# Optimization experiments

Measured on AMD Instinct MI355X. Metric: run time of the kernel, lower is better.

Reference implementation:

```python
import jax, jax.numpy as jnp
import numpy as np

N_NODES = 50000
N_EDGES = 800000
IN_F = 128
OUT_F = 64
ALPHA = 0.2  # LeakyReLU negative slope


def setup_inputs() -> dict:
    key = jax.random.key(0)
    k_h, k_e, k_w, k_b, k_a = jax.random.split(key, 5)
    h = jax.random.normal(k_h, (N_NODES, IN_F), dtype=jnp.float32)
    adj = jax.random.randint(k_e, (2, N_EDGES), 0, N_NODES, dtype=jnp.int64)
    # Linear(in_features, out_features): weight [out, in], bias [out]
    W_w = jax.random.normal(k_w, (OUT_F, IN_F), dtype=jnp.float32) * (1.0 / np.sqrt(IN_F))
    W_b = jax.random.normal(k_b, (OUT_F,), dtype=jnp.float32) * 0.01
    a = jax.random.normal(k_a, (1, 2 * OUT_F), dtype=jnp.float32) * (1.0 / np.sqrt(2 * OUT_F))
    return {"h": h, "adj": adj, "W_w": W_w, "W_b": W_b, "a": a}


def reference(h, adj, W_w, W_b, a):
    N = h.shape[0]
    F_out = W_w.shape[0]
    inv_sqrt_f = 1.0 / float(np.sqrt(F_out))

    data = h @ W_w.T + W_b                      # [N, F_out]
    src, dst = adj[0], adj[1]

    # a @ [data[src] || data[dst]]^T  == (data @ a_src)[src] + (data @ a_dst)[dst]
    a_src, a_dst = a[0, :F_out], a[0, F_out:]
    score = (data @ a_src)[src] + (data @ a_dst)[dst]       # [E]
    edge_e = jnp.exp(jax.nn.leaky_relu(score, ALPHA) * inv_sqrt_f)

    # sparse rowsum over source rows (duplicate edges sum, matching COO semantics)
    rowsum = jax.ops.segment_sum(edge_e, src, num_segments=N)  # [N]
    row_zero = rowsum == 0.0
    rowsum = jnp.where(row_zero, 1.0, rowsum)

    # sparse mm: sum_e edge_e * data[dst] into row src; zero rows get a unit self-loop
    h_prime = jax.ops.segment_sum(edge_e[:, None] * data[dst], src, num_segments=N)
    h_prime = h_prime + row_zero[:, None].astype(data.dtype) * data
    return h_prime / rowsum[:, None]
```

## Files before the change

kernel.cpp:

```cpp
#include <hip/hip_runtime.h>
#include <math.h>

#define IN_F 128
#define OUT_F 64
#define ALPHA 0.2f
#define INV_SQRT_F 0.125f
#define CAP 64
#define BINSH 7
#define BINSZ 128
#define CAPB 4096

typedef _Float16 h8  __attribute__((ext_vector_type(8)));
typedef float    f4  __attribute__((ext_vector_type(4)));

__device__ __forceinline__ float edge_w(float sc) {
    float lr = sc > 0.f ? sc : ALPHA * sc;
    return __expf(lr * INV_SQRT_F);
}

__device__ __forceinline__ h8 cvt8(float4 a, float4 b) {
    h8 r;
    r[0] = (_Float16)a.x; r[1] = (_Float16)a.y;
    r[2] = (_Float16)a.z; r[3] = (_Float16)a.w;
    r[4] = (_Float16)b.x; r[5] = (_Float16)b.y;
    r[6] = (_Float16)b.z; r[7] = (_Float16)b.w;
    return r;
}

__global__ __launch_bounds__(256) void k_p1(
    const float* __restrict__ h, const float* __restrict__ W,
    const float* __restrict__ b, const float* __restrict__ a,
    const int* __restrict__ src, const int* __restrict__ dst,
    int* __restrict__ gcur, unsigned* __restrict__ pk,
    _Float16* __restrict__ data_h,
    float* __restrict__ s_src, float* __restrict__ s_dst,
    int n_nodes, int n_edges, int g_lin)
{
    __shared__ int hist[512];
    __shared__ int off[512];
    const int tid = threadIdx.x;

    if ((int)blockIdx.x >= g_lin) {
        const int nbins = (n_nodes + BINSZ - 1) >> BINSH;
        const int e0 = ((int)blockIdx.x - g_lin) * 4096 + tid * 16;

        for (int i = tid; i < nbins; i += 256) hist[i] = 0;
        __syncthreads();

        int s[16], d[16];
        const bool full = (e0 + 16 <= n_edges);
        if (full) {
            #pragma unroll
            for (int c = 0; c < 4; ++c) {
                int4 s4 = *(const int4*)&src[e0 + c * 4];
                int4 d4 = *(const int4*)&dst[e0 + c * 4];
                s[c*4+0] = s4.x; s[c*4+1] = s4.y; s[c*4+2] = s4.z; s[c*4+3] = s4.w;
                d[c*4+0] = d4.x; d[c*4+1] = d4.y; d[c*4+2] = d4.z; d[c*4+3] = d4.w;
            }
            #pragma unroll
            for (int i = 0; i < 16; ++i)
                atomicAdd(&hist[s[i] >> BINSH], 1);
        } else {
            #pragma unroll
            for (int i = 0; i < 16; ++i) {
                int e = e0 + i;
                s[i] = (e < n_edges) ? src[e] : -1;
                d[i] = (e < n_edges) ? dst[e] : 0;
                if (s[i] >= 0) atomicAdd(&hist[s[i] >> BINSH], 1);
            }
        }
        __syncthreads();

        for (int i = tid; i < nbins; i += 256) {
            int c = hist[i];
            off[i] = (c > 0) ? atomicAdd(&gcur[i], c) : 0;
            hist[i] = 0;
        }
        __syncthreads();

        #pragma unroll
        for (int i = 0; i < 16; ++i) {
            if (s[i] < 0) continue;
            int bin = s[i] >> BINSH;
            int r = atomicAdd(&hist[bin], 1);
            int p = off[bin] + r;
            if (p < CAPB)
                pk[(size_t)bin * CAPB + p] =
                    ((unsigned)(s[i] & (BINSZ - 1)) << 16) | (unsigned)d[i];
        }
        return;
    }

    const int node0 = (int)blockIdx.x * 64;
    const int wv  = tid >> 6;
    const int lane = tid & 63;
    const int q   = lane >> 4;
    const int col = lane & 15;
    const int r0  = wv * 16;

    const int arow = min(node0 + r0 + col, n_nodes - 1);
    const float* __restrict__ hrow = h + (size_t)arow * IN_F;

    f4 acc[4] = {{0.f,0.f,0.f,0.f},{0.f,0.f,0.f,0.f},
                 {0.f,0.f,0.f,0.f},{0.f,0.f,0.f,0.f}};
    #pragma unroll
    for (int kk = 0; kk < 4; ++kk) {
        const int ko = kk * 32 + q * 8;
        float4 ha = *(const float4*)&hrow[ko];
        float4 hb = *(const float4*)&hrow[ko + 4];
        h8 av = cvt8(ha, hb);
        #pragma unroll
        for (int ct = 0; ct < 4; ++ct) {
            const float* wrow = W + (size_t)(ct * 16 + col) * IN_F + ko;
            float4 wa = *(const float4*)&wrow[0];
            float4 wb = *(const float4*)&wrow[4];
            h8 bv = cvt8(wa, wb);
            acc[ct] = __builtin_amdgcn_mfma_f32_16x16x32_f16(av, bv, acc[ct], 0, 0, 0);
        }
    }

    float bb[4], as_[4], ad_[4];
    #pragma unroll
    for (int ct = 0; ct < 4; ++ct) {
        bb[ct]  = b[ct * 16 + col];
        as_[ct] = a[ct * 16 + col];
        ad_[ct] = a[OUT_F + ct * 16 + col];
    }
    #pragma unroll
    for (int reg = 0; reg < 4; ++reg) {
        int n = node0 + r0 + q * 4 + reg;
        float vv[4], ps = 0.f, pd = 0.f;
        #pragma unroll
        for (int ct = 0; ct < 4; ++ct) {
            float v = acc[ct][reg] + bb[ct];
            vv[ct] = v;
            ps = fmaf(v, as_[ct], ps);
            pd = fmaf(v, ad_[ct], pd);
        }
        #pragma unroll
        for (int m = 1; m <= 8; m <<= 1) {
            ps += __shfl_xor(ps, m, 64);
            pd += __shfl_xor(pd, m, 64);
        }
        if (n < n_nodes) {
            size_t base = (size_t)n * OUT_F + col;
            #pragma unroll
            for (int ct = 0; ct < 4; ++ct)
                data_h[base + ct * 16] = (_Float16)vv[ct];
            if (col == 0) { s_src[n] = ps; s_dst[n] = pd; }
        }
    }
}

__global__ __launch_bounds__(256) void k_p2(
    const unsigned* __restrict__ pk, const int* __restrict__ gcur,
    unsigned short* __restrict__ db, int* __restrict__ cnt, int n_nodes)
{
    __shared__ unsigned short dbl[BINSZ * CAP];
    __shared__ int lcnt[BINSZ];
    const int b = blockIdx.x, tid = threadIdx.x;

    for (int i = tid; i < BINSZ; i += 256) lcnt[i] = 0;
    __syncthreads();

    const int ecnt = min(gcur[b], CAPB);
    for (int i = tid; i < ecnt; i += 256) {
        unsigned v = pk[(size_t)b * CAPB + i];
        int sl = (int)(v >> 16);
        int r = atomicAdd(&lcnt[sl], 1);
        if (r < CAP) dbl[sl * CAP + r] = (unsigned short)(v & 0xffffu);
    }
    __syncthreads();

    const int sbase = b * BINSZ;
    for (int i = tid; i < BINSZ; i += 256) {
        int s = sbase + i;
        if (s < n_nodes) cnt[s] = lcnt[i];
    }
    unsigned* dbu = (unsigned*)db;
    const unsigned* dbl32 = (const unsigned*)dbl;
    const size_t obase = (size_t)b * (BINSZ * CAP / 2);
    for (int i = tid; i < BINSZ * CAP / 2; i += 256)
        __builtin_nontemporal_store(dbl32[i], &dbu[obase + i]);
}

__global__ __launch_bounds__(256) void k_gather(
    const unsigned short* __restrict__ db, const int* __restrict__ cnt,
    const float* __restrict__ s_src, const float* __restrict__ s_dst,
    const _Float16* __restrict__ data_h, float* __restrict__ out, int n_nodes)
{
    const int wv = threadIdx.x >> 6, lane = threadIdx.x & 63;
    const int n = blockIdx.x * 4 + wv;
    if (n >= n_nodes) return;
    const int cn = min(cnt[n], CAP);
    const int g  = lane >> 3;
    const int fl = lane & 7;
    const float ssrc = s_src[n];
    const size_t bbase = (size_t)n * CAP;

    float ac[8] = {0.f,0.f,0.f,0.f,0.f,0.f,0.f,0.f};
    float rs = 0.f;
    int t = 0;
    for (; t + 16 <= cn; t += 16) {
        int d0 = (int)db[bbase + t + g];
        int d1 = (int)db[bbase + t + 8 + g];
        float w0 = edge_w(ssrc + s_dst[d0]);
        float w1 = edge_w(ssrc + s_dst[d1]);
        h8 x0 = *(const h8*)&data_h[(size_t)d0 * OUT_F + 8 * fl];
        h8 x1 = *(const h8*)&data_h[(size_t)d1 * OUT_F + 8 * fl];
        #pragma unroll
        for (int i = 0; i < 8; ++i) ac[i] = fmaf(w0, (float)x0[i], ac[i]);
        #pragma unroll
        for (int i = 0; i < 8; ++i) ac[i] = fmaf(w1, (float)x1[i], ac[i]);
        rs += w0 + w1;
    }
    for (; t + 8 <= cn; t += 8) {
        int d0 = (int)db[bbase + t + g];
        float w0 = edge_w(ssrc + s_dst[d0]);
        h8 x0 = *(const h8*)&data_h[(size_t)d0 * OUT_F + 8 * fl];
        #pragma unroll
        for (int i = 0; i < 8; ++i) ac[i] = fmaf(w0, (float)x0[i], ac[i]);
        rs += w0;
    }
    const int rem = cn - t;
    if (g < rem) {
        int d0 = (int)db[bbase + t + g];
        float w0 = edge_w(ssrc + s_dst[d0]);
        h8 x0 = *(const h8*)&data_h[(size_t)d0 * OUT_F + 8 * fl];
        #pragma unroll
        for (int i = 0; i < 8; ++i) ac[i] = fmaf(w0, (float)x0[i], ac[i]);
        rs += w0;
    }
    #pragma unroll
    for (int m = 8; m <= 32; m <<= 1) {
        #pragma unroll
        for (int i = 0; i < 8; ++i) ac[i] += __shfl_xor(ac[i], m, 64);
        rs += __shfl_xor(rs, m, 64);
    }

    if (g == 0) {
        size_t o = (size_t)n * OUT_F + 8 * fl;
        f4 r0, r1;
        if (rs == 0.f) {
            h8 xv = *(const h8*)&data_h[o];
            r0[0] = (float)xv[0]; r0[1] = (float)xv[1];
            r0[2] = (float)xv[2]; r0[3] = (float)xv[3];
            r1[0] = (float)xv[4]; r1[1] = (float)xv[5];
            r1[2] = (float)xv[6]; r1[3] = (float)xv[7];
        } else {
            float inv = 1.f / rs;
            r0[0] = ac[0] * inv; r0[1] = ac[1] * inv;
            r0[2] = ac[2] * inv; r0[3] = ac[3] * inv;
            r1[0] = ac[4] * inv; r1[1] = ac[5] * inv;
            r1[2] = ac[6] * inv; r1[3] = ac[7] * inv;
        }
        __builtin_nontemporal_store(r0, (f4*)&out[o]);
        __builtin_nontemporal_store(r1, (f4*)&out[o + 4]);
    }
}

extern "C" void kernel_launch(void* const* d_in, const int* in_sizes, int n_in,
                              void* d_out, int out_size, void* d_ws, size_t ws_size,
                              hipStream_t stream)
{
    const float* h   = (const float*)d_in[0];
    const int*   adj = (const int*)  d_in[1];
    const float* W   = (const float*)d_in[2];
    const float* b   = (const float*)d_in[3];
    const float* a   = (const float*)d_in[4];
    float* out = (float*)d_out;

    const int n_nodes = in_sizes[0] / IN_F;
    const int n_edges = in_sizes[1] / 2;
    const int* src = adj;
    const int* dst = adj + n_edges;
    const int nbins = (n_nodes + BINSZ - 1) >> BINSH;

    char* p = (char*)d_ws;
    _Float16*       data_h = (_Float16*)p;       p += (size_t)n_nodes * OUT_F * 2;
    unsigned short* db     = (unsigned short*)p; p += (size_t)nbins * BINSZ * CAP * 2;
    unsigned*       pk     = (unsigned*)p;       p += (size_t)nbins * CAPB * 4;
    float*          s_src  = (float*)p;          p += (size_t)n_nodes * 4;
    float*          s_dst  = (float*)p;          p += (size_t)n_nodes * 4;
    int*            cnt    = (int*)p;            p += (size_t)n_nodes * 4;
    int*            gcur   = (int*)p;            p += (size_t)nbins * 4;

    (void)hipMemsetAsync(gcur, 0, (size_t)nbins * sizeof(int), stream);

    const int g_lin = (n_nodes + 63) / 64;
    const int g_p1  = (n_edges + 4095) / 4096;
    k_p1<<<g_lin + g_p1, 256, 0, stream>>>(
        h, W, b, a, src, dst, gcur, pk, data_h, s_src, s_dst,
        n_nodes, n_edges, g_lin);

    k_p2<<<nbins, 256, 0, stream>>>(pk, gcur, db, cnt, n_nodes);

    k_gather<<<(n_nodes + 3) / 4, 256, 0, stream>>>(
        db, cnt, s_src, s_dst, data_h, out, n_nodes);
}
```

Measured before the change: 132.4 us.

## Fuse bin scatter and gather into one kernel with LDS-resident adjacency

Merges the per-bin bucketing kernel and the per-node gather kernel so each 1024-thread block builds its bin's adjacency lists in shared memory and immediately aggregates the 128 nodes from there. This removes the global write and reread of the padded neighbor list and count arrays and one kernel launch. The linear-projection blocks now stage W converted to fp16 in LDS, and edge-binning blocks are ordered first. The risk is reduced parallelism in the gather phase, since there are only a few hundred large blocks processing nodes serially per wave.

Measured after the change: 124.8 us. 5.7% less time.

```diff
diff --git a/kernel.cpp b/kernel.cpp
--- a/kernel.cpp
+++ b/kernel.cpp
@@ -9,6 +9,7 @@
 #define BINSH 7
 #define BINSZ 128
 #define CAPB 4096
+#define HS 136
 
 typedef _Float16 h8  __attribute__((ext_vector_type(8)));
 typedef float    f4  __attribute__((ext_vector_type(4)));
@@ -34,15 +35,16 @@
     int* __restrict__ gcur, unsigned* __restrict__ pk,
     _Float16* __restrict__ data_h,
     float* __restrict__ s_src, float* __restrict__ s_dst,
-    int n_nodes, int n_edges, int g_lin)
+    int n_nodes, int n_edges, int g_p1)
 {
+    __shared__ _Float16 wsh[OUT_F * HS];
     __shared__ int hist[512];
     __shared__ int off[512];
     const int tid = threadIdx.x;
 
-    if ((int)blockIdx.x >= g_lin) {
+    if ((int)blockIdx.x < g_p1) {
         const int nbins = (n_nodes + BINSZ - 1) >> BINSH;
-        const int e0 = ((int)blockIdx.x - g_lin) * 4096 + tid * 16;
+        const int e0 = (int)blockIdx.x * 4096 + tid * 16;
 
         for (int i = tid; i < nbins; i += 256) hist[i] = 0;
         __syncthreads();
@@ -91,7 +93,16 @@
         return;
     }
 
-    const int node0 = (int)blockIdx.x * 64;
+    const int node0 = ((int)blockIdx.x - g_p1) * 64;
+
+    for (int i = tid * 8; i < OUT_F * IN_F; i += 2048) {
+        int f = i >> 7, k = i & 127;
+        float4 va = *(const float4*)&W[i];
+        float4 vb = *(const float4*)&W[i + 4];
+        *(h8*)&wsh[f * HS + k] = cvt8(va, vb);
+    }
+    __syncthreads();
+
     const int wv  = tid >> 6;
     const int lane = tid & 63;
     const int q   = lane >> 4;
@@ -111,10 +122,7 @@
         h8 av = cvt8(ha, hb);
         #pragma unroll
         for (int ct = 0; ct < 4; ++ct) {
-            const float* wrow = W + (size_t)(ct * 16 + col) * IN_F + ko;
-            float4 wa = *(const float4*)&wrow[0];
-            float4 wb = *(const float4*)&wrow[4];
-            h8 bv = cvt8(wa, wb);
+            h8 bv = *(const h8*)&wsh[(ct * 16 + col) * HS + ko];
             acc[ct] = __builtin_amdgcn_mfma_f32_16x16x32_f16(av, bv, acc[ct], 0, 0, 0);
         }
     }
@@ -152,110 +160,99 @@
     }
 }
 
-__global__ __launch_bounds__(256) void k_p2(
+__global__ __launch_bounds__(1024) void k_bin(
     const unsigned* __restrict__ pk, const int* __restrict__ gcur,
-    unsigned short* __restrict__ db, int* __restrict__ cnt, int n_nodes)
+    const float* __restrict__ s_src, const float* __restrict__ s_dst,
+    const _Float16* __restrict__ data_h, float* __restrict__ out, int n_nodes)
 {
     __shared__ unsigned short dbl[BINSZ * CAP];
     __shared__ int lcnt[BINSZ];
-    const int b = blockIdx.x, tid = threadIdx.x;
-
-    for (int i = tid; i < BINSZ; i += 256) lcnt[i] = 0;
+    const int bin = blockIdx.x, tid = threadIdx.x;
+
+    for (int i = tid; i < BINSZ; i += 1024) lcnt[i] = 0;
     __syncthreads();
 
-    const int ecnt = min(gcur[b], CAPB);
-    for (int i = tid; i < ecnt; i += 256) {
-        unsigned v = pk[(size_t)b * CAPB + i];
+    const int ecnt = min(gcur[bin], CAPB);
+    for (int i = tid; i < ecnt; i += 1024) {
+        unsigned v = pk[(size_t)bin * CAPB + i];
         int sl = (int)(v >> 16);
         int r = atomicAdd(&lcnt[sl], 1);
         if (r < CAP) dbl[sl * CAP + r] = (unsigned short)(v & 0xffffu);
     }
     __syncthreads();
 
-    const int sbase = b * BINSZ;
-    for (int i = tid; i < BINSZ; i += 256) {
-        int s = sbase + i;
-        if (s < n_nodes) cnt[s] = lcnt[i];
-    }
-    unsigned* dbu = (unsigned*)db;
-    const unsigned* dbl32 = (const unsigned*)dbl;
-    const size_t obase = (size_t)b * (BINSZ * CAP / 2);
-    for (int i = tid; i < BINSZ * CAP / 2; i += 256)
-        __builtin_nontemporal_store(dbl32[i], &dbu[obase + i]);
-}
-
-__global__ __launch_bounds__(256) void k_gather(
-    const unsigned short* __restrict__ db, const int* __restrict__ cnt,
-    const float* __restrict__ s_src, const float* __restrict__ s_dst,
-    const _Float16* __restrict__ data_h, float* __restrict__ out, int n_nodes)
-{
-    const int wv = threadIdx.x >> 6, lane = threadIdx.x & 63;
-    const int n = blockIdx.x * 4 + wv;
-    if (n >= n_nodes) return;
-    const int cn = min(cnt[n], CAP);
+    const int wv = tid >> 6, lane = tid & 63;
     const int g  = lane >> 3;
     const int fl = lane & 7;
-    const float ssrc = s_src[n];
-    const size_t bbase = (size_t)n * CAP;
-
-    float ac[8] = {0.f,0.f,0.f,0.f,0.f,0.f,0.f,0.f};
-    float rs = 0.f;
-    int t = 0;
-    for (; t + 16 <= cn; t += 16) {
-        int d0 = (int)db[bbase + t + g];
-        int d1 = (int)db[bbase + t + 8 + g];
-        float w0 = edge_w(ssrc + s_dst[d0]);
-        float w1 = edge_w(ssrc + s_dst[d1]);
-        h8 x0 = *(const h8*)&data_h[(size_t)d0 * OUT_F + 8 * fl];
-        h8 x1 = *(const h8*)&data_h[(size_t)d1 * OUT_F + 8 * fl];
-        #pragma unroll
-        for (int i = 0; i < 8; ++i) ac[i] = fmaf(w0, (float)x0[i], ac[i]);
-        #pragma unroll
-        for (int i = 0; i < 8; ++i) ac[i] = fmaf(w1, (float)x1[i], ac[i]);
-        rs += w0 + w1;
-    }
-    for (; t + 8 <= cn; t += 8) {
-        int d0 = (int)db[bbase + t + g];
-        float w0 = edge_w(ssrc + s_dst[d0]);
-        h8 x0 = *(const h8*)&data_h[(size_t)d0 * OUT_F + 8 * fl];
-        #pragma unroll
-        for (int i = 0; i < 8; ++i) ac[i] = fmaf(w0, (float)x0[i], ac[i]);
-        rs += w0;
-    }
-    const int rem = cn - t;
-    if (g < rem) {
-        int d0 = (int)db[bbase + t + g];
-        float w0 = edge_w(ssrc + s_dst[d0]);
-        h8 x0 = *(const h8*)&data_h[(size_t)d0 * OUT_F + 8 * fl];
-        #pragma unroll
-        for (int i = 0; i < 8; ++i) ac[i] = fmaf(w0, (float)x0[i], ac[i]);
-        rs += w0;
-    }
-    #pragma unroll
-    for (int m = 8; m <= 32; m <<= 1) {
-        #pragma unroll
-        for (int i = 0; i < 8; ++i) ac[i] += __shfl_xor(ac[i], m, 64);
-        rs += __shfl_xor(rs, m, 64);
-    }
-
-    if (g == 0) {
-        size_t o = (size_t)n * OUT_F + 8 * fl;
-        f4 r0, r1;
-        if (rs == 0.f) {
-            h8 xv = *(const h8*)&data_h[o];
-            r0[0] = (float)xv[0]; r0[1] = (float)xv[1];
-            r0[2] = (float)xv[2]; r0[3] = (float)xv[3];
-            r1[0] = (float)xv[4]; r1[1] = (float)xv[5];
-            r1[2] = (float)xv[6]; r1[3] = (float)xv[7];
-        } else {
-            float inv = 1.f / rs;
-            r0[0] = ac[0] * inv; r0[1] = ac[1] * inv;
-            r0[2] = ac[2] * inv; r0[3] = ac[3] * inv;
-            r1[0] = ac[4] * inv; r1[1] = ac[5] * inv;
-            r1[2] = ac[6] * inv; r1[3] = ac[7] * inv;
-        }
-        __builtin_nontemporal_store(r0, (f4*)&out[o]);
-        __builtin_nontemporal_store(r1, (f4*)&out[o + 4]);
+
+    #pragma unroll 1
+    for (int ni = 0; ni < 8; ++ni) {
+        const int nl = wv * 8 + ni;
+        const int n = bin * BINSZ + nl;
+        if (n >= n_nodes) break;
+        const int cn = min(lcnt[nl], CAP);
+        const float ssrc = s_src[n];
+        const int bbase = nl * CAP;
+
+        float ac[8] = {0.f,0.f,0.f,0.f,0.f,0.f,0.f,0.f};
+        float rs = 0.f;
+        int t = 0;
+        for (; t + 16 <= cn; t += 16) {
+            int d0 = (int)dbl[bbase + t + g];
+            int d1 = (int)dbl[bbase + t + 8 + g];
+            float w0 = edge_w(ssrc + s_dst[d0]);
+            float w1 = edge_w(ssrc + s_dst[d1]);
+            h8 x0 = *(const h8*)&data_h[(size_t)d0 * OUT_F + 8 * fl];
+            h8 x1 = *(const h8*)&data_h[(size_t)d1 * OUT_F + 8 * fl];
+            #pragma unroll
+            for (int i = 0; i < 8; ++i) ac[i] = fmaf(w0, (float)x0[i], ac[i]);
+            #pragma unroll
+            for (int i = 0; i < 8; ++i) ac[i] = fmaf(w1, (float)x1[i], ac[i]);
+            rs += w0 + w1;
+        }
+        for (; t + 8 <= cn; t += 8) {
+            int d0 = (int)dbl[bbase + t + g];
+            float w0 = edge_w(ssrc + s_dst[d0]);
+            h8 x0 = *(const h8*)&data_h[(size_t)d0 * OUT_F + 8 * fl];
+            #pragma unroll
+            for (int i = 0; i < 8; ++i) ac[i] = fmaf(w0, (float)x0[i], ac[i]);
+            rs += w0;
+        }
+        const int rem = cn - t;
+        if (g < rem) {
+            int d0 = (int)dbl[bbase + t + g];
+            float w0 = edge_w(ssrc + s_dst[d0]);
+            h8 x0 = *(const h8*)&data_h[(size_t)d0 * OUT_F + 8 * fl];
+            #pragma unroll
+            for (int i = 0; i < 8; ++i) ac[i] = fmaf(w0, (float)x0[i], ac[i]);
+            rs += w0;
+        }
+        #pragma unroll
+        for (int m = 8; m <= 32; m <<= 1) {
+            #pragma unroll
+            for (int i = 0; i < 8; ++i) ac[i] += __shfl_xor(ac[i], m, 64);
+            rs += __shfl_xor(rs, m, 64);
+        }
+
+        if (g == 0) {
+            size_t o = (size_t)n * OUT_F + 8 * fl;
+            f4 r0, r1;
+            if (rs == 0.f) {
+                h8 xv = *(const h8*)&data_h[o];
+                r0[0] = (float)xv[0]; r0[1] = (float)xv[1];
+                r0[2] = (float)xv[2]; r0[3] = (float)xv[3];
+                r1[0] = (float)xv[4]; r1[1] = (float)xv[5];
+                r1[2] = (float)xv[6]; r1[3] = (float)xv[7];
+            } else {
+                float inv = 1.f / rs;
+                r0[0] = ac[0] * inv; r0[1] = ac[1] * inv;
+                r0[2] = ac[2] * inv; r0[3] = ac[3] * inv;
+                r1[0] = ac[4] * inv; r1[1] = ac[5] * inv;
+                r1[2] = ac[6] * inv; r1[3] = ac[7] * inv;
+            }
+            __builtin_nontemporal_store(r0, (f4*)&out[o]);
+            __builtin_nontemporal_store(r1, (f4*)&out[o + 4]);
+        }
     }
 }
 
@@ -278,23 +275,19 @@
 
     char* p = (char*)d_ws;
     _Float16*       data_h = (_Float16*)p;       p += (size_t)n_nodes * OUT_F * 2;
-    unsigned short* db     = (unsigned short*)p; p += (size_t)nbins * BINSZ * CAP * 2;
     unsigned*       pk     = (unsigned*)p;       p += (size_t)nbins * CAPB * 4;
     float*          s_src  = (float*)p;          p += (size_t)n_nodes * 4;
     float*          s_dst  = (float*)p;          p += (size_t)n_nodes * 4;
-    int*            cnt    = (int*)p;            p += (size_t)n_nodes * 4;
     int*            gcur   = (int*)p;            p += (size_t)nbins * 4;
 
     (void)hipMemsetAsync(gcur, 0, (size_t)nbins * sizeof(int), stream);
 
+    const int g_p1  = (n_edges + 4095) / 4096;
     const int g_lin = (n_nodes + 63) / 64;
-    const int g_p1  = (n_edges + 4095) / 4096;
-    k_p1<<<g_lin + g_p1, 256, 0, stream>>>(
+    k_p1<<<g_p1 + g_lin, 256, 0, stream>>>(
         h, W, b, a, src, dst, gcur, pk, data_h, s_src, s_dst,
-        n_nodes, n_edges, g_lin);
-
-    k_p2<<<nbins, 256, 0, stream>>>(pk, gcur, db, cnt, n_nodes);
-
-    k_gather<<<(n_nodes + 3) / 4, 256, 0, stream>>>(
-        db, cnt, s_src, s_dst, data_h, out, n_nodes);
-}
+        n_nodes, n_edges, g_p1);
+
+    k_bin<<<nbins, 1024, 0, stream>>>(
+        pk, gcur, s_src, s_dst, data_h, out, n_nodes);
+}
```
